# Performance work log

Hardware: AMD Instinct MI355X
Metric: run time of the kernel (lower is better)

The kernel has to match this reference:

```python
import jax, jax.numpy as jnp
import numpy as np

B, T, D = 4, 8192, 1024

def setup_inputs() -> dict:
    key = jax.random.key(0)
    k1, k2, k3 = jax.random.split(key, 3)
    x = jax.random.normal(k1, (B, T, D), dtype=jnp.float32)
    decay = jax.random.normal(k2, (D,), dtype=jnp.float32)
    freq = jax.random.normal(k3, (D,), dtype=jnp.float32)
    return {"x": x, "decay": decay, "freq": freq}

def reference(x, decay, freq):
    Bb, Tt, Dd = x.shape
    t = jnp.arange(Tt, dtype=jnp.float32)  # [T]
    # kernel: [T, D]
    k = jnp.exp(-jnp.abs(decay)[None, :] * t[:, None]) * jnp.cos(freq[None, :] * t[:, None])
    n_fft = 2 * Tt
    x_f = jnp.fft.rfft(x.astype(jnp.float32), n=n_fft, axis=1)   # [B, T+1, D] complex
    k_f = jnp.fft.rfft(k, n=n_fft, axis=0)                        # [T+1, D] complex
    y = jnp.fft.irfft(x_f * k_f[None, :, :], n=n_fft, axis=1)    # [B, 2T, D]
    return y[:, :Tt, :].astype(x.dtype)
```

## Files before the change

kernel.cpp:

```cpp
#include <hip/hip_runtime.h>
#include <cmath>

#define BB 4
#define TT 8192
#define DD 1024
#define DBLK 16
#define NDB (DD/DBLK)
#define NCHAIN (BB*NDB)
#define CL 1024
#define NITER (TT/CL)
#define NTHR 512
#define NPART (NTHR/DBLK)
#define PLEN (CL/NPART)


__global__ __launch_bounds__(NTHR, 2) void fftconv_persist(
    const float* __restrict__ x, const float* __restrict__ decay,
    const float* __restrict__ freq, float* __restrict__ y)
{
    __shared__ float  tile[2][CL*DBLK];
    __shared__ float2 Ssub[NPART][DBLK];
    __shared__ float2 eoff[NPART][DBLK];
    __shared__ float2 HB[DBLK];

    const int tid  = threadIdx.x;
    const int l16  = tid & 15;
    const int part = tid >> 4;
    const int wv   = tid >> 6;
    const int wl   = tid & 63;
    const int bid  = blockIdx.x;
    const int chain = (bid & 7)*32 + (bid >> 3);
    const int dblk  = chain & (NDB-1);
    const int b     = chain >> 6;
    const int d     = dblk*DBLK + l16;

    const float a = fabsf(decay[d]);
    const float w = freq[d];
    float s_, c_, e;
    e = expf(-a);                    sincosf(w, &s_, &c_);
    const float rr = e*c_, ri = e*s_;
    e = expf(-a*(float)PLEN);        sincosf(w*(float)PLEN, &s_, &c_);
    const float Msr = e*c_, Msi = e*s_;
    e = expf(-a*(float)CL);          sincosf(w*(float)CL, &s_, &c_);
    const float Mcr = e*c_, Mci = e*s_;
    e = expf(-a*(float)(PLEN*part)); sincosf(w*(float)(PLEN*part), &s_, &c_);
    const float Mpr = e*c_, Mpi = e*s_;

    const float* xch = x + (size_t)b*TT*DD + dblk*DBLK;
    float*       ych = y + (size_t)b*TT*DD + dblk*DBLK;

    auto stage = [&](int k, int buf) {
        const float* xc = xch + (size_t)(k*CL)*DD;
        const int rofs = wl >> 2;
        const int gofs = (wl & 3) << 2;
#pragma unroll
        for (int i = 0; i < 8; ++i) {
            const int r0 = (wv*8 + i)*16;
            __builtin_amdgcn_global_load_lds(
                (const __attribute__((address_space(1))) void*)
                    (xc + (size_t)(r0 + rofs)*DD + gofs),
                (__attribute__((address_space(3))) void*)&tile[buf][r0*DBLK],
                16, 0, 0);
        }
    };

    float Hr = 0.f, Hi = 0.f;

    stage(0, 0);
    asm volatile("s_waitcnt vmcnt(0)" ::: "memory");
    __builtin_amdgcn_s_barrier();
    __builtin_amdgcn_sched_barrier(0);

    for (int k = 0; k < NITER; ++k) {
        const int cur = k & 1;

        float hRr[PLEN];
        {
            float hr = 0.f, hi = 0.f;
            const int rowbase = part*PLEN;
#pragma unroll
            for (int t = 0; t < PLEN; ++t) {
                float xv = tile[cur][(rowbase + t)*DBLK + l16];
                float nr = fmaf(rr, hr, fmaf(-ri, hi, xv));
                hi = fmaf(rr, hi, ri*hr);
                hr = nr;
                hRr[t] = hr;
            }
            Ssub[part][l16] = make_float2(hr, hi);
        }
        asm volatile("s_waitcnt lgkmcnt(0)" ::: "memory");
        __builtin_amdgcn_s_barrier();
        __builtin_amdgcn_sched_barrier(0);

        if (k + 1 < NITER) stage(k + 1, cur ^ 1);

        if (tid < DBLK) {
            float Lr = 0.f, Li = 0.f;
#pragma unroll
            for (int p = 0; p < NPART; ++p) {
                eoff[p][l16] = make_float2(Lr, Li);
                float2 Sp = Ssub[p][l16];
                float nr = fmaf(Msr, Lr, fmaf(-Msi, Li, Sp.x));
                Li = fmaf(Msr, Li, fmaf(Msi, Lr, Sp.y));
                Lr = nr;
            }
            HB[l16] = make_float2(Hr, Hi);
            float nHr = fmaf(Mcr, Hr, fmaf(-Mci, Hi, Lr));
            Hi = fmaf(Mcr, Hi, fmaf(Mci, Hr, Li));
            Hr = nHr;
        }
        asm volatile("s_waitcnt lgkmcnt(0)" ::: "memory");
        __builtin_amdgcn_s_barrier();
        __builtin_amdgcn_sched_barrier(0);

        {
            float2 Hp = HB[l16];
            float2 eo = eoff[part][l16];
            float Sr = eo.x + (Mpr*Hp.x - Mpi*Hp.y);
            float Si = eo.y + (Mpr*Hp.y + Mpi*Hp.x);
            float wr = rr*Sr - ri*Si;
            float wi = rr*Si + ri*Sr;
            float* yp = ych + (size_t)(k*CL + part*PLEN)*DD + l16;
#pragma unroll
            for (int t = 0; t < PLEN; ++t) {
                yp[(size_t)t*DD] = hRr[t] + wr;
                float nwr = rr*wr - ri*wi;
                wi = rr*wi + ri*wr;
                wr = nwr;
            }
        }

        if (k + 1 < NITER) {
            asm volatile("s_waitcnt vmcnt(32)" ::: "memory");
            __builtin_amdgcn_s_barrier();
            __builtin_amdgcn_sched_barrier(0);
        }
    }
}

extern "C" void kernel_launch(void* const* d_in, const int* in_sizes, int n_in,
                              void* d_out, int out_size, void* d_ws, size_t ws_size,
                              hipStream_t stream) {
    const float* x     = (const float*)d_in[0];
    const float* decay = (const float*)d_in[1];
    const float* freq  = (const float*)d_in[2];
    float*       y     = (float*)d_out;

    fftconv_persist<<<NCHAIN, NTHR, 0, stream>>>(x, decay, freq, y);
}
```

Before: 50.77 us.

## Halve channel block width to double grid and add XOR-swizzled LDS staging

Cuts the per-block channel group from 16 to 8 and the chunk length from 1024 to 512, with 256 threads per block, so the grid doubles to 512 persistent blocks. The global-to-LDS staging is rewritten for 8-wide rows and uses an XOR swizzle on source rows, matched on the read side, to spread LDS bank accesses. More blocks should help fill the CUs, at the cost of narrower 32-byte row segments for global loads and stores and more loop iterations per chain.

Result: slower. 60.94 us (+20.0%).

```diff
diff --git a/kernel.cpp b/kernel.cpp
--- a/kernel.cpp
+++ b/kernel.cpp
@@ -4,12 +4,12 @@
 #define BB 4
 #define TT 8192
 #define DD 1024
-#define DBLK 16
+#define DBLK 8
 #define NDB (DD/DBLK)
 #define NCHAIN (BB*NDB)
-#define CL 1024
+#define CL 512
 #define NITER (TT/CL)
-#define NTHR 512
+#define NTHR 256
 #define NPART (NTHR/DBLK)
 #define PLEN (CL/NPART)
 
@@ -24,15 +24,15 @@
     __shared__ float2 HB[DBLK];
 
     const int tid  = threadIdx.x;
-    const int l16  = tid & 15;
-    const int part = tid >> 4;
+    const int l8   = tid & 7;
+    const int part = tid >> 3;
     const int wv   = tid >> 6;
     const int wl   = tid & 63;
     const int bid  = blockIdx.x;
-    const int chain = (bid & 7)*32 + (bid >> 3);
+    const int chain = (bid & 7)*64 + (bid >> 3);
     const int dblk  = chain & (NDB-1);
-    const int b     = chain >> 6;
-    const int d     = dblk*DBLK + l16;
+    const int b     = chain >> 7;
+    const int d     = dblk*DBLK + l8;
 
     const float a = fabsf(decay[d]);
     const float w = freq[d];
@@ -51,20 +51,21 @@
 
     auto stage = [&](int k, int buf) {
         const float* xc = xch + (size_t)(k*CL)*DD;
-        const int rofs = wl >> 2;
-        const int gofs = (wl & 3) << 2;
 #pragma unroll
-        for (int i = 0; i < 8; ++i) {
-            const int r0 = (wv*8 + i)*16;
+        for (int i = 0; i < 4; ++i) {
+            const int base_u = wv*256 + i*64;
+            const int uidx   = base_u + wl;
+            const int usrc   = uidx ^ (((uidx >> 5) & 3) << 1);
             __builtin_amdgcn_global_load_lds(
                 (const __attribute__((address_space(1))) void*)
-                    (xc + (size_t)(r0 + rofs)*DD + gofs),
-                (__attribute__((address_space(3))) void*)&tile[buf][r0*DBLK],
+                    (xc + (size_t)(usrc >> 1)*DD + ((usrc & 1) << 2)),
+                (__attribute__((address_space(3))) void*)&tile[buf][base_u << 2],
                 16, 0, 0);
         }
     };
 
     float Hr = 0.f, Hi = 0.f;
+    const int cxor = (part & 3) << 3;
 
     stage(0, 0);
     asm volatile("s_waitcnt vmcnt(0)" ::: "memory");
@@ -77,16 +78,16 @@
         float hRr[PLEN];
         {
             float hr = 0.f, hi = 0.f;
-            const int rowbase = part*PLEN;
+            const int rowbase = part*PLEN*DBLK;
 #pragma unroll
             for (int t = 0; t < PLEN; ++t) {
-                float xv = tile[cur][(rowbase + t)*DBLK + l16];
+                float xv = tile[cur][(rowbase + (t << 3) + l8) ^ cxor];
                 float nr = fmaf(rr, hr, fmaf(-ri, hi, xv));
                 hi = fmaf(rr, hi, ri*hr);
                 hr = nr;
                 hRr[t] = hr;
             }
-            Ssub[part][l16] = make_float2(hr, hi);
+            Ssub[part][l8] = make_float2(hr, hi);
         }
         asm volatile("s_waitcnt lgkmcnt(0)" ::: "memory");
         __builtin_amdgcn_s_barrier();
@@ -98,13 +99,13 @@
             float Lr = 0.f, Li = 0.f;
 #pragma unroll
             for (int p = 0; p < NPART; ++p) {
-                eoff[p][l16] = make_float2(Lr, Li);
-                float2 Sp = Ssub[p][l16];
+                eoff[p][l8] = make_float2(Lr, Li);
+                float2 Sp = Ssub[p][l8];
                 float nr = fmaf(Msr, Lr, fmaf(-Msi, Li, Sp.x));
                 Li = fmaf(Msr, Li, fmaf(Msi, Lr, Sp.y));
                 Lr = nr;
             }
-            HB[l16] = make_float2(Hr, Hi);
+            HB[l8] = make_float2(Hr, Hi);
             float nHr = fmaf(Mcr, Hr, fmaf(-Mci, Hi, Lr));
             Hi = fmaf(Mcr, Hi, fmaf(Mci, Hr, Li));
             Hr = nHr;
@@ -114,13 +115,13 @@
         __builtin_amdgcn_sched_barrier(0);
 
         {
-            float2 Hp = HB[l16];
-            float2 eo = eoff[part][l16];
+            float2 Hp = HB[l8];
+            float2 eo = eoff[part][l8];
             float Sr = eo.x + (Mpr*Hp.x - Mpi*Hp.y);
             float Si = eo.y + (Mpr*Hp.y + Mpi*Hp.x);
             float wr = rr*Sr - ri*Si;
             float wi = rr*Si + ri*Sr;
-            float* yp = ych + (size_t)(k*CL + part*PLEN)*DD + l16;
+            float* yp = ych + (size_t)(k*CL + part*PLEN)*DD + l8;
 #pragma unroll
             for (int t = 0; t < PLEN; ++t) {
                 yp[(size_t)t*DD] = hRr[t] + wr;
@@ -131,7 +132,7 @@
         }
 
         if (k + 1 < NITER) {
-            asm volatile("s_waitcnt vmcnt(32)" ::: "memory");
+            asm volatile("s_waitcnt vmcnt(16)" ::: "memory");
             __builtin_amdgcn_s_barrier();
             __builtin_amdgcn_sched_barrier(0);
         }
```
